# Optimization experiments

Hardware: AMD Instinct MI355X
Metric: run time of the kernel (lower is better)

Reference implementation:

```python
import jax, jax.numpy as jnp
import numpy as np

FIELD = 7  # field_size


def _conv1x1(x, w):
    # x: [b,c,h,w], w: [c_out,c_in] (1x1 conv, no bias)
    return jnp.einsum('bchw,oc->bohw', x, w)


def _patches(x, f):
    # torch unfold with 'same' padding: output [b, c*f*f, h, w], channel-major
    # (feature index = c*f*f + kh*f + kw), matching KAIR extract_image_patches
    # layout for odd f / stride 1 (symmetric pad (f-1)//2).
    return jax.lax.conv_general_dilated_patches(
        x, filter_shape=(f, f), window_strides=(1, 1), padding='SAME',
        dimension_numbers=('NCHW', 'OIHW', 'NCHW'))


def setup_inputs() -> dict:
    key = jax.random.key(0)
    k0, k1, k2, k3, k4 = jax.random.split(key, 5)
    c, ci = 256, 128
    b, h, w = 4, 64, 64
    s = 1.0 / np.sqrt(c)
    si = 1.0 / np.sqrt(ci)
    return {
        'x': jax.random.normal(k0, (b, c, h, w), dtype=jnp.float32),
        'w_phi': jax.random.normal(k1, (ci, c), dtype=jnp.float32) * s,
        'w_theta': jax.random.normal(k2, (ci, c), dtype=jnp.float32) * s,
        'w_g': jax.random.normal(k3, (ci, c), dtype=jnp.float32) * s,
        'w_mask': jax.random.normal(k4, (c, ci), dtype=jnp.float32) * si,
    }


def reference(x, w_phi, w_theta, w_g, w_mask):
    b, c, h, w = x.shape
    ci = w_phi.shape[0]
    f = FIELD
    kk = f * f

    x_phi = _conv1x1(x, w_phi)      # [b,ci,h,w]
    x_g = _conv1x1(x, w_g)          # [b,ci,h,w]
    x_theta = _conv1x1(x, w_theta)  # [b,ci,h,w]

    # theta: unsqueeze(-2) then permute(0,2,4,3,1) -> [b,h,w,1,ci]
    q = jnp.transpose(x_theta, (0, 2, 3, 1))[:, :, :, None, :]

    # phi patches: [b, ci*kk, h, w] reshaped (row-major, faithful to torch
    # reshape of the unfold output) to [b,h,w,ci,kk]
    p_phi = _patches(x_phi, f).reshape(b, h, w, ci, kk)
    scores = jnp.matmul(q, p_phi)                 # [b,h,w,1,kk]
    attn = jax.nn.softmax(scores, axis=1)         # softmax over dim=1 (h), faithful

    p_g = _patches(x_g, f).reshape(b, h, w, kk, ci)
    out = jnp.matmul(attn, p_g)                   # [b,h,w,1,ci]

    # permute(0,4,3,1,2).view(b,ci,h,w)
    y = jnp.transpose(out, (0, 4, 3, 1, 2)).reshape(b, ci, h, w)
    mask = _conv1x1(y, w_mask)                    # [b,c,h,w]
    return mask + x
```

## Files before the change

kernel.cpp:

```cpp
#include <hip/hip_runtime.h>


#define PLANE    5040
#define A_BATCH  645120

typedef __attribute__((ext_vector_type(8))) short short8;
typedef __attribute__((ext_vector_type(4))) float floatx4;

__device__ __forceinline__ float bf2f(unsigned short u) {
    union { unsigned int i; float f; } v; v.i = ((unsigned int)u) << 16; return v.f;
}
__device__ __forceinline__ unsigned short f2bf(float f) {
    union { float f; unsigned int i; } v; v.f = f;
    unsigned int r = v.i + 0x7FFFu + ((v.i >> 16) & 1u);
    return (unsigned short)(r >> 16);
}

__global__ __launch_bounds__(256) void prep_kernel(
    const float* __restrict__ x,
    const float* __restrict__ w_phi,
    const float* __restrict__ w_theta,
    const float* __restrict__ w_g,
    const float* __restrict__ w_mask,
    unsigned short* __restrict__ xp_hi,
    unsigned short* __restrict__ xp_lo,
    unsigned short* __restrict__ w3p_hi,
    unsigned short* __restrict__ w3p_lo,
    unsigned short* __restrict__ wmp_hi,
    unsigned short* __restrict__ wmp_lo,
    uint4* __restrict__ zero_region)
{
    const int tid = threadIdx.x;
    const int bx = blockIdx.x;

    if (bx < 1024) {
        const int b  = bx >> 8;
        const int kt = (bx >> 6) & 3;
        const int pt = bx & 63;
        __shared__ float tile[64][65];
        #pragma unroll
        for (int i = 0; i < 16; ++i) {
            int lin = tid + i * 256;
            int kk = lin >> 6, pp = lin & 63;
            tile[kk][pp] = x[(b * 256 + kt * 64 + kk) * 4096 + pt * 64 + pp];
        }
        __syncthreads();
        #pragma unroll
        for (int i = 0; i < 16; ++i) {
            int lin = tid + i * 256;
            int frag = lin >> 9;
            int idx  = lin & 511;
            int kbL  = frag >> 2;
            int ptL  = frag & 3;
            int j    = idx & 7;
            int n    = (idx >> 3) & 15;
            int quad = idx >> 7;
            float f = tile[kbL * 32 + quad * 8 + j][ptL * 16 + n];
            unsigned short h = f2bf(f);
            int addr = ((b * 8 + kt * 2 + kbL) * 256 + pt * 4 + ptL) * 512 + idx;
            xp_hi[addr] = h;
            xp_lo[addr] = f2bf(f - bf2f(h));
        }
    } else {
        const int wid = (bx - 1024) * 256 + tid;
        for (int e = wid; e < 98304; e += 32768) {
            int frag = e >> 9;
            int idx  = e & 511;
            int nt16 = frag >> 3, kb = frag & 7;
            int j = idx & 7, m = (idx >> 3) & 15, quad = idx >> 7;
            int n = nt16 * 16 + m;
            int k = kb * 32 + quad * 8 + j;
            float v = (n < 128) ? w_phi[n * 256 + k]
                    : (n < 256) ? w_theta[(n - 128) * 256 + k]
                                : w_g[(n - 256) * 256 + k];
            unsigned short h = f2bf(v);
            w3p_hi[e] = h;
            w3p_lo[e] = f2bf(v - bf2f(h));
        }
        {
            int e = wid;
            int frag = e >> 9;
            int idx  = e & 511;
            int ot16 = frag >> 2, kb = frag & 3;
            int j = idx & 7, m = (idx >> 3) & 15, quad = idx >> 7;
            float v = w_mask[(ot16 * 16 + m) * 128 + kb * 32 + quad * 8 + j];
            unsigned short h = f2bf(v);
            wmp_hi[e] = h;
            wmp_lo[e] = f2bf(v - bf2f(h));
        }
        const uint4 z = make_uint4(0u, 0u, 0u, 0u);
        for (int i = wid; i < 645120; i += 32768) zero_region[i] = z;
    }
}

__global__ __launch_bounds__(256) void conv3_mfma_kernel(
    const unsigned short* __restrict__ xp_hi,
    const unsigned short* __restrict__ xp_lo,
    const unsigned short* __restrict__ w3p_hi,
    const unsigned short* __restrict__ w3p_lo,
    unsigned short* __restrict__ A_phi,
    unsigned short* __restrict__ theta_bf,
    unsigned short* __restrict__ A_g)
{
    const int tid = threadIdx.x;
    const int w   = tid >> 6;
    const int ln  = tid & 63;
    const int lm  = ln & 15;
    const int quad = ln >> 4;
    const int bx = blockIdx.x;
    const int nt = blockIdx.y;
    const int b  = blockIdx.z;
    const int nt16a = nt * 8 + w;
    const int nt16b = nt * 8 + 4 + w;
    const int lnofs = ln * 8;

    floatx4 accA[4] = {{0.f,0.f,0.f,0.f},{0.f,0.f,0.f,0.f},
                       {0.f,0.f,0.f,0.f},{0.f,0.f,0.f,0.f}};
    floatx4 accB[4] = {{0.f,0.f,0.f,0.f},{0.f,0.f,0.f,0.f},
                       {0.f,0.f,0.f,0.f},{0.f,0.f,0.f,0.f}};

    #pragma unroll
    for (int kb = 0; kb < 8; ++kb) {
        const int aoffA = (nt16a * 8 + kb) * 512 + lnofs;
        const int aoffB = (nt16b * 8 + kb) * 512 + lnofs;
        const int boff  = ((b * 8 + kb) * 256 + bx * 4) * 512 + lnofs;
        short8 ahA = *reinterpret_cast<const short8*>(w3p_hi + aoffA);
        short8 alA = *reinterpret_cast<const short8*>(w3p_lo + aoffA);
        short8 ahB = *reinterpret_cast<const short8*>(w3p_hi + aoffB);
        short8 alB = *reinterpret_cast<const short8*>(w3p_lo + aoffB);
        short8 bh[4], bl[4];
        #pragma unroll
        for (int ct = 0; ct < 4; ++ct) {
            bh[ct] = *reinterpret_cast<const short8*>(xp_hi + boff + ct * 512);
            bl[ct] = *reinterpret_cast<const short8*>(xp_lo + boff + ct * 512);
        }
        #pragma unroll
        for (int ct = 0; ct < 4; ++ct) {
            accA[ct] = __builtin_amdgcn_mfma_f32_16x16x32_bf16(ahA, bh[ct], accA[ct], 0, 0, 0);
            accA[ct] = __builtin_amdgcn_mfma_f32_16x16x32_bf16(ahA, bl[ct], accA[ct], 0, 0, 0);
            accA[ct] = __builtin_amdgcn_mfma_f32_16x16x32_bf16(alA, bh[ct], accA[ct], 0, 0, 0);
            accB[ct] = __builtin_amdgcn_mfma_f32_16x16x32_bf16(ahB, bh[ct], accB[ct], 0, 0, 0);
            accB[ct] = __builtin_amdgcn_mfma_f32_16x16x32_bf16(ahB, bl[ct], accB[ct], 0, 0, 0);
            accB[ct] = __builtin_amdgcn_mfma_f32_16x16x32_bf16(alB, bh[ct], accB[ct], 0, 0, 0);
        }
    }

    const int py = bx;
    if (nt == 1) {
        #pragma unroll
        for (int ct = 0; ct < 4; ++ct) {
            const int p = bx * 64 + ct * 16 + lm;
            #pragma unroll
            for (int reg = 0; reg < 4; ++reg) {
                const int r = w * 16 + quad * 4 + reg;
                theta_bf[(b * 4096 + p) * 128 + r]      = f2bf(accA[ct][reg]);
                theta_bf[(b * 4096 + p) * 128 + r + 64] = f2bf(accB[ct][reg]);
            }
        }
    } else {
        unsigned short* __restrict__ A = (nt == 0) ? A_phi : A_g;
        #pragma unroll
        for (int ct = 0; ct < 4; ++ct) {
            const int pxx = ct * 16 + lm;
            #pragma unroll
            for (int reg = 0; reg < 4; ++reg) {
                const int r = w * 16 + quad * 4 + reg;
                A[b * A_BATCH + r * PLANE + (py + 3) * 72 + pxx + 4] =
                    f2bf(accA[ct][reg]);
                A[b * A_BATCH + (r + 64) * PLANE + (py + 3) * 72 + pxx + 4] =
                    f2bf(accB[ct][reg]);
            }
        }
    }
}

__global__ __launch_bounds__(256) void scores_kernel(
    const unsigned short* __restrict__ Apad,
    const unsigned short* __restrict__ theta_bf,
    float* __restrict__ scores)
{
    const int w  = threadIdx.x >> 6;
    const int ln = threadIdx.x & 63;
    const int s  = blockIdx.x * 4 + w;
    const int b  = blockIdx.y;

    __shared__ float th[4][128];
    {
        const unsigned short* tb = theta_bf + (b * 4096 + s) * 128;
        th[w][ln]      = bf2f(tb[ln]);
        th[w][ln + 64] = bf2f(tb[ln + 64]);
    }
    __syncthreads();

    const unsigned short* __restrict__ Ab = Apad + b * A_BATCH;

    const int base  = s * 6272;
    const int ch_lo = base >> 12;
    const unsigned B1 = (unsigned)(ch_lo + 1) << 12;
    const unsigned B2 = (unsigned)(ch_lo + 2) << 12;
    const int d1 = (int)B1 - base;
    const int d2 = d1 + 4096;

    int A1 = d1 / 49;
    int A2 = (d1 + 48) / 49;
    int C1 = d2 / 49;        if (C1 > 128) C1 = 128;
    int C2 = (d2 + 48) / 49; if (C2 > 128) C2 = 128;

    unsigned OFFv[3];
    #pragma unroll
    for (int i = 0; i < 3; ++i) {
        int ch = ch_lo + i;
        int c0 = ch / 49; if (c0 > 127) c0 = 127;
        int rr = ch - c0 * 49;
        int kh = rr / 7;
        int kw = rr - kh * 7;
        OFFv[i] = (unsigned)(c0 * PLANE + kh * 72 + kw + 1);
    }

    unsigned F = (unsigned)(base + ln);
    float acc = 0.f;

    {
        const unsigned OFF_ = OFFv[0];
        #pragma unroll 4
        for (int cc = 0; cc < A1; ++cc) {
            unsigned p = F & 4095u;
            unsigned a = OFF_ + p + ((p >> 6) << 3);
            acc = fmaf(th[w][cc], bf2f(Ab[a]), acc);
            F += 49u;
        }
    }
    for (int cc = A1; cc < A2; ++cc) {
        unsigned OFF_ = (F >= B1) ? OFFv[1] : OFFv[0];
        unsigned p = F & 4095u;
        unsigned a = OFF_ + p + ((p >> 6) << 3);
        acc = fmaf(th[w][cc], bf2f(Ab[a]), acc);
        F += 49u;
    }
    {
        const unsigned OFF_ = OFFv[1];
        #pragma unroll 4
        for (int cc = A2; cc < C1; ++cc) {
            unsigned p = F & 4095u;
            unsigned a = OFF_ + p + ((p >> 6) << 3);
            acc = fmaf(th[w][cc], bf2f(Ab[a]), acc);
            F += 49u;
        }
    }
    for (int cc = C1; cc < C2; ++cc) {
        unsigned OFF_ = (F >= B2) ? OFFv[2] : OFFv[1];
        unsigned p = F & 4095u;
        unsigned a = OFF_ + p + ((p >> 6) << 3);
        acc = fmaf(th[w][cc], bf2f(Ab[a]), acc);
        F += 49u;
    }
    {
        const unsigned OFF_ = OFFv[2];
        #pragma unroll 4
        for (int cc = C2; cc < 128; ++cc) {
            unsigned p = F & 4095u;
            unsigned a = OFF_ + p + ((p >> 6) << 3);
            acc = fmaf(th[w][cc], bf2f(Ab[a]), acc);
            F += 49u;
        }
    }

    if (ln < 49) scores[(b * 4096 + s) * 64 + ln] = acc;
}

__global__ __launch_bounds__(256) void softmax_stats_kernel(
    const float* __restrict__ scores,
    float* __restrict__ m_arr,
    float* __restrict__ inv_arr)
{
    const int b = blockIdx.x >> 6;
    const int j = blockIdx.x & 63;
    const int tid = threadIdx.x;
    const int wv = tid >> 6;
    const int ln = tid & 63;

    __shared__ float tile[64][52];

    #pragma unroll
    for (int it = 0; it < 16; ++it) {
        int i = it * 4 + wv;
        if (ln < 49) tile[i][ln] = scores[(b * 4096 + i * 64 + j) * 64 + ln];
    }
    __syncthreads();

    if (tid < 49) {
        float m = -3.4e38f;
        #pragma unroll 8
        for (int i = 0; i < 64; ++i) m = fmaxf(m, tile[i][tid]);
        float sum = 0.f;
        #pragma unroll 8
        for (int i = 0; i < 64; ++i) sum += __expf(tile[i][tid] - m);
        m_arr[(b * 64 + j) * 49 + tid]   = m;
        inv_arr[(b * 64 + j) * 49 + tid] = 1.f / sum;
    }
}

__global__ __launch_bounds__(256) void aggregate_kernel(
    const float* __restrict__ scores,
    const float* __restrict__ m_arr,
    const float* __restrict__ inv_arr,
    const unsigned short* __restrict__ Apad,
    unsigned short* __restrict__ y_p)
{
    const int pix = threadIdx.x >> 7;
    const int cc  = threadIdx.x & 127;
    const int s   = blockIdx.x * 2 + pix;
    const int b   = blockIdx.y;

    __shared__ float at[2][52];
    if (cc < 49) {
        const int j = s & 63;
        float sc = scores[(b * 4096 + s) * 64 + cc];
        float m  = m_arr[(b * 64 + j) * 49 + cc];
        float iv = inv_arr[(b * 64 + j) * 49 + cc];
        at[pix][cc] = __expf(sc - m) * iv;
    }
    __syncthreads();

    const unsigned short* __restrict__ Ab = Apad + b * A_BATCH;

    const int base  = s * 6272;
    const int ch_lo = base >> 12;
    const unsigned B1 = (unsigned)(ch_lo + 1) << 12;
    const unsigned B2 = (unsigned)(ch_lo + 2) << 12;
    const int d1 = (int)B1 - base;
    const int d2 = d1 + 4096;

    int A1 = d1 >> 7;
    int A2 = (d1 + 127) >> 7;
    int C1 = d2 >> 7;          if (C1 > 49) C1 = 49;
    int C2 = (d2 + 127) >> 7;  if (C2 > 49) C2 = 49;
    if (A1 > 49) A1 = 49;
    if (A2 > 49) A2 = 49;

    unsigned OFFv[3];
    #pragma unroll
    for (int i = 0; i < 3; ++i) {
        int ch = ch_lo + i;
        int c0 = ch / 49; if (c0 > 127) c0 = 127;
        int rr = ch - c0 * 49;
        int kh = rr / 7;
        int kw = rr - kh * 7;
        OFFv[i] = (unsigned)(c0 * PLANE + kh * 72 + kw + 1);
    }

    unsigned F = (unsigned)(base + cc);
    float acc = 0.f;

    {
        const unsigned OFF_ = OFFv[0];
        #pragma unroll 4
        for (int t = 0; t < A1; ++t) {
            unsigned p = F & 4095u;
            unsigned a = OFF_ + p + ((p >> 6) << 3);
            acc = fmaf(at[pix][t], bf2f(Ab[a]), acc);
            F += 128u;
        }
    }
    for (int t = A1; t < A2; ++t) {
        unsigned OFF_ = (F >= B1) ? OFFv[1] : OFFv[0];
        unsigned p = F & 4095u;
        unsigned a = OFF_ + p + ((p >> 6) << 3);
        acc = fmaf(at[pix][t], bf2f(Ab[a]), acc);
        F += 128u;
    }
    {
        const unsigned OFF_ = OFFv[1];
        #pragma unroll 4
        for (int t = A2; t < C1; ++t) {
            unsigned p = F & 4095u;
            unsigned a = OFF_ + p + ((p >> 6) << 3);
            acc = fmaf(at[pix][t], bf2f(Ab[a]), acc);
            F += 128u;
        }
    }
    for (int t = C1; t < C2; ++t) {
        unsigned OFF_ = (F >= B2) ? OFFv[2] : OFFv[1];
        unsigned p = F & 4095u;
        unsigned a = OFF_ + p + ((p >> 6) << 3);
        acc = fmaf(at[pix][t], bf2f(Ab[a]), acc);
        F += 128u;
    }
    {
        const unsigned OFF_ = OFFv[2];
        for (int t = C2; t < 49; ++t) {
            unsigned p = F & 4095u;
            unsigned a = OFF_ + p + ((p >> 6) << 3);
            acc = fmaf(at[pix][t], bf2f(Ab[a]), acc);
            F += 128u;
        }
    }

    const int kb = cc >> 5, k32 = cc & 31;
    const int quad = k32 >> 3, j = k32 & 7;
    const int pt16 = s >> 4, n = s & 15;
    y_p[((b * 4 + kb) * 256 + pt16) * 512 + (quad * 16 + n) * 8 + j] = f2bf(acc);
}

__global__ __launch_bounds__(256) void maskconv_mfma_kernel(
    const float* __restrict__ x,
    const unsigned short* __restrict__ wmp_hi,
    const unsigned short* __restrict__ wmp_lo,
    const unsigned short* __restrict__ y_p,
    float* __restrict__ out)
{
    const int tid = threadIdx.x;
    const int w   = tid >> 6;
    const int ln  = tid & 63;
    const int lm  = ln & 15;
    const int quad = ln >> 4;
    const int bx = blockIdx.x;
    const int ot = blockIdx.y;
    const int b  = blockIdx.z;
    const int ot16a = ot * 8 + w;
    const int ot16b = ot * 8 + 4 + w;
    const int lnofs = ln * 8;

    floatx4 accA[4] = {{0.f,0.f,0.f,0.f},{0.f,0.f,0.f,0.f},
                       {0.f,0.f,0.f,0.f},{0.f,0.f,0.f,0.f}};
    floatx4 accB[4] = {{0.f,0.f,0.f,0.f},{0.f,0.f,0.f,0.f},
                       {0.f,0.f,0.f,0.f},{0.f,0.f,0.f,0.f}};

    #pragma unroll
    for (int kb = 0; kb < 4; ++kb) {
        const int aoffA = (ot16a * 4 + kb) * 512 + lnofs;
        const int aoffB = (ot16b * 4 + kb) * 512 + lnofs;
        const int boff  = ((b * 4 + kb) * 256 + bx * 4) * 512 + lnofs;
        short8 ahA = *reinterpret_cast<const short8*>(wmp_hi + aoffA);
        short8 alA = *reinterpret_cast<const short8*>(wmp_lo + aoffA);
        short8 ahB = *reinterpret_cast<const short8*>(wmp_hi + aoffB);
        short8 alB = *reinterpret_cast<const short8*>(wmp_lo + aoffB);
        short8 bf[4];
        #pragma unroll
        for (int ct = 0; ct < 4; ++ct)
            bf[ct] = *reinterpret_cast<const short8*>(y_p + boff + ct * 512);
        #pragma unroll
        for (int ct = 0; ct < 4; ++ct) {
            accA[ct] = __builtin_amdgcn_mfma_f32_16x16x32_bf16(ahA, bf[ct], accA[ct], 0, 0, 0);
            accA[ct] = __builtin_amdgcn_mfma_f32_16x16x32_bf16(alA, bf[ct], accA[ct], 0, 0, 0);
            accB[ct] = __builtin_amdgcn_mfma_f32_16x16x32_bf16(ahB, bf[ct], accB[ct], 0, 0, 0);
            accB[ct] = __builtin_amdgcn_mfma_f32_16x16x32_bf16(alB, bf[ct], accB[ct], 0, 0, 0);
        }
    }

    #pragma unroll
    for (int ct = 0; ct < 4; ++ct) {
        const int p = bx * 64 + ct * 16 + lm;
        #pragma unroll
        for (int reg = 0; reg < 4; ++reg) {
            const int oA = ot * 128 + w * 16 + quad * 4 + reg;
            const int ofsA = (b * 256 + oA) * 4096 + p;
            out[ofsA] = accA[ct][reg] + x[ofsA];
            const int ofsB = ofsA + 64 * 4096;
            out[ofsB] = accB[ct][reg] + x[ofsB];
        }
    }
}

extern "C" void kernel_launch(void* const* d_in, const int* in_sizes, int n_in,
                              void* d_out, int out_size, void* d_ws, size_t ws_size,
                              hipStream_t stream) {
    const float* x       = (const float*)d_in[0];
    const float* w_phi   = (const float*)d_in[1];
    const float* w_theta = (const float*)d_in[2];
    const float* w_g     = (const float*)d_in[3];
    const float* w_mask  = (const float*)d_in[4];

    float* out_f = (float*)d_out;

    unsigned short* ws_u  = (unsigned short*)d_ws;
    unsigned short* A_phi = ws_u;
    unsigned short* A_g   = ws_u + 2580480;
    unsigned short* y_p   = ws_u + 5160960;
    unsigned short* th_u  = ws_u + 7258112;
    float*          sc_f  = (float*)(ws_u + 9355264);
    unsigned short* xph   = ws_u + 11452416;
    unsigned short* xpl   = ws_u + 15646720;
    unsigned short* w3ph  = ws_u + 19841024;
    unsigned short* w3pl  = ws_u + 19939328;
    unsigned short* wmph  = ws_u + 20037632;
    unsigned short* wmpl  = ws_u + 20070400;
    float*          m_f   = (float*)(ws_u + 20103168);
    float*          inv_f = (float*)(ws_u + 20128256);

    hipLaunchKernelGGL(prep_kernel, dim3(1152), dim3(256), 0, stream,
                       x, w_phi, w_theta, w_g, w_mask,
                       xph, xpl, w3ph, w3pl, wmph, wmpl, (uint4*)A_phi);
    hipLaunchKernelGGL(conv3_mfma_kernel, dim3(64, 3, 4), dim3(256), 0, stream,
                       xph, xpl, w3ph, w3pl, A_phi, th_u, A_g);
    hipLaunchKernelGGL(scores_kernel, dim3(1024, 4), dim3(256), 0, stream,
                       A_phi, th_u, sc_f);
    hipLaunchKernelGGL(softmax_stats_kernel, dim3(256), dim3(256), 0, stream,
                       sc_f, m_f, inv_f);
    hipLaunchKernelGGL(aggregate_kernel, dim3(2048, 4), dim3(256), 0, stream,
                       sc_f, m_f, inv_f, A_g, y_p);
    hipLaunchKernelGGL(maskconv_mfma_kernel, dim3(64, 2, 4), dim3(256), 0, stream,
                       x, wmph, wmpl, y_p, out_f);
}
```

Measured before the change: 177.6 us.

## Compute all three projections per block to reuse loaded input tiles

The three-projection 1x1 conv kernel now has each block compute phi, theta and g together for 32 pixels, instead of one projection for 64 pixels. Each loaded x tile (hi/lo bf16 split) is reused across all three weight sets, so activation reads drop to a third. The grid changes from 64x3x4 to 128x4 blocks. The cost is more weight loads per block and more accumulator registers (12 floatx4 instead of 8).

```diff
diff --git a/kernel.cpp b/kernel.cpp
--- a/kernel.cpp
+++ b/kernel.cpp
@@ -108,68 +108,73 @@
     const int lm  = ln & 15;
     const int quad = ln >> 4;
     const int bx = blockIdx.x;
-    const int nt = blockIdx.y;
-    const int b  = blockIdx.z;
-    const int nt16a = nt * 8 + w;
-    const int nt16b = nt * 8 + 4 + w;
+    const int b  = blockIdx.y;
     const int lnofs = ln * 8;
 
-    floatx4 accA[4] = {{0.f,0.f,0.f,0.f},{0.f,0.f,0.f,0.f},
-                       {0.f,0.f,0.f,0.f},{0.f,0.f,0.f,0.f}};
-    floatx4 accB[4] = {{0.f,0.f,0.f,0.f},{0.f,0.f,0.f,0.f},
-                       {0.f,0.f,0.f,0.f},{0.f,0.f,0.f,0.f}};
+    floatx4 acc[3][2][2];
+    #pragma unroll
+    for (int nt = 0; nt < 3; ++nt)
+        #pragma unroll
+        for (int tl = 0; tl < 2; ++tl)
+            #pragma unroll
+            for (int ct = 0; ct < 2; ++ct)
+                acc[nt][tl][ct] = (floatx4){0.f, 0.f, 0.f, 0.f};
 
     #pragma unroll
     for (int kb = 0; kb < 8; ++kb) {
-        const int aoffA = (nt16a * 8 + kb) * 512 + lnofs;
-        const int aoffB = (nt16b * 8 + kb) * 512 + lnofs;
-        const int boff  = ((b * 8 + kb) * 256 + bx * 4) * 512 + lnofs;
-        short8 ahA = *reinterpret_cast<const short8*>(w3p_hi + aoffA);
-        short8 alA = *reinterpret_cast<const short8*>(w3p_lo + aoffA);
-        short8 ahB = *reinterpret_cast<const short8*>(w3p_hi + aoffB);
-        short8 alB = *reinterpret_cast<const short8*>(w3p_lo + aoffB);
-        short8 bh[4], bl[4];
-        #pragma unroll
-        for (int ct = 0; ct < 4; ++ct) {
+        const int boff = ((b * 8 + kb) * 256 + bx * 2) * 512 + lnofs;
+        short8 bh[2], bl[2];
+        #pragma unroll
+        for (int ct = 0; ct < 2; ++ct) {
             bh[ct] = *reinterpret_cast<const short8*>(xp_hi + boff + ct * 512);
             bl[ct] = *reinterpret_cast<const short8*>(xp_lo + boff + ct * 512);
         }
         #pragma unroll
-        for (int ct = 0; ct < 4; ++ct) {
-            accA[ct] = __builtin_amdgcn_mfma_f32_16x16x32_bf16(ahA, bh[ct], accA[ct], 0, 0, 0);
-            accA[ct] = __builtin_amdgcn_mfma_f32_16x16x32_bf16(ahA, bl[ct], accA[ct], 0, 0, 0);
-            accA[ct] = __builtin_amdgcn_mfma_f32_16x16x32_bf16(alA, bh[ct], accA[ct], 0, 0, 0);
-            accB[ct] = __builtin_amdgcn_mfma_f32_16x16x32_bf16(ahB, bh[ct], accB[ct], 0, 0, 0);
-            accB[ct] = __builtin_amdgcn_mfma_f32_16x16x32_bf16(ahB, bl[ct], accB[ct], 0, 0, 0);
-            accB[ct] = __builtin_amdgcn_mfma_f32_16x16x32_bf16(alB, bh[ct], accB[ct], 0, 0, 0);
-        }
-    }
-
-    const int py = bx;
-    if (nt == 1) {
-        #pragma unroll
-        for (int ct = 0; ct < 4; ++ct) {
-            const int p = bx * 64 + ct * 16 + lm;
+        for (int nt = 0; nt < 3; ++nt) {
+            const int nt16a = nt * 8 + w;
+            const int nt16b = nt * 8 + 4 + w;
+            const int aoffA = (nt16a * 8 + kb) * 512 + lnofs;
+            const int aoffB = (nt16b * 8 + kb) * 512 + lnofs;
+            short8 ahA = *reinterpret_cast<const short8*>(w3p_hi + aoffA);
+            short8 alA = *reinterpret_cast<const short8*>(w3p_lo + aoffA);
+            short8 ahB = *reinterpret_cast<const short8*>(w3p_hi + aoffB);
+            short8 alB = *reinterpret_cast<const short8*>(w3p_lo + aoffB);
             #pragma unroll
-            for (int reg = 0; reg < 4; ++reg) {
-                const int r = w * 16 + quad * 4 + reg;
-                theta_bf[(b * 4096 + p) * 128 + r]      = f2bf(accA[ct][reg]);
-                theta_bf[(b * 4096 + p) * 128 + r + 64] = f2bf(accB[ct][reg]);
+            for (int ct = 0; ct < 2; ++ct) {
+                acc[nt][0][ct] = __builtin_amdgcn_mfma_f32_16x16x32_bf16(ahA, bh[ct], acc[nt][0][ct], 0, 0, 0);
+                acc[nt][0][ct] = __builtin_amdgcn_mfma_f32_16x16x32_bf16(ahA, bl[ct], acc[nt][0][ct], 0, 0, 0);
+                acc[nt][0][ct] = __builtin_amdgcn_mfma_f32_16x16x32_bf16(alA, bh[ct], acc[nt][0][ct], 0, 0, 0);
+                acc[nt][1][ct] = __builtin_amdgcn_mfma_f32_16x16x32_bf16(ahB, bh[ct], acc[nt][1][ct], 0, 0, 0);
+                acc[nt][1][ct] = __builtin_amdgcn_mfma_f32_16x16x32_bf16(ahB, bl[ct], acc[nt][1][ct], 0, 0, 0);
+                acc[nt][1][ct] = __builtin_amdgcn_mfma_f32_16x16x32_bf16(alB, bh[ct], acc[nt][1][ct], 0, 0, 0);
             }
         }
-    } else {
-        unsigned short* __restrict__ A = (nt == 0) ? A_phi : A_g;
-        #pragma unroll
-        for (int ct = 0; ct < 4; ++ct) {
-            const int pxx = ct * 16 + lm;
-            #pragma unroll
-            for (int reg = 0; reg < 4; ++reg) {
-                const int r = w * 16 + quad * 4 + reg;
-                A[b * A_BATCH + r * PLANE + (py + 3) * 72 + pxx + 4] =
-                    f2bf(accA[ct][reg]);
-                A[b * A_BATCH + (r + 64) * PLANE + (py + 3) * 72 + pxx + 4] =
-                    f2bf(accB[ct][reg]);
-            }
+    }
+
+    const int py   = bx >> 1;
+    const int px32 = (bx & 1) * 32;
+
+    #pragma unroll
+    for (int ct = 0; ct < 2; ++ct) {
+        const int p = bx * 32 + ct * 16 + lm;
+        #pragma unroll
+        for (int reg = 0; reg < 4; ++reg) {
+            const int r = w * 16 + quad * 4 + reg;
+            theta_bf[(b * 4096 + p) * 128 + r]      = f2bf(acc[1][0][ct][reg]);
+            theta_bf[(b * 4096 + p) * 128 + r + 64] = f2bf(acc[1][1][ct][reg]);
+        }
+    }
+    #pragma unroll
+    for (int ct = 0; ct < 2; ++ct) {
+        const int pxx = px32 + ct * 16 + lm;
+        const int pbase = (py + 3) * 72 + pxx + 4;
+        #pragma unroll
+        for (int reg = 0; reg < 4; ++reg) {
+            const int r = w * 16 + quad * 4 + reg;
+            A_phi[b * A_BATCH + r * PLANE + pbase]        = f2bf(acc[0][0][ct][reg]);
+            A_phi[b * A_BATCH + (r + 64) * PLANE + pbase] = f2bf(acc[0][1][ct][reg]);
+            A_g[b * A_BATCH + r * PLANE + pbase]          = f2bf(acc[2][0][ct][reg]);
+            A_g[b * A_BATCH + (r + 64) * PLANE + pbase]   = f2bf(acc[2][1][ct][reg]);
         }
     }
 }
@@ -491,7 +496,7 @@
     hipLaunchKernelGGL(prep_kernel, dim3(1152), dim3(256), 0, stream,
                        x, w_phi, w_theta, w_g, w_mask,
                        xph, xpl, w3ph, w3pl, wmph, wmpl, (uint4*)A_phi);
-    hipLaunchKernelGGL(conv3_mfma_kernel, dim3(64, 3, 4), dim3(256), 0, stream,
+    hipLaunchKernelGGL(conv3_mfma_kernel, dim3(128, 4), dim3(256), 0, stream,
                        xph, xpl, w3ph, w3pl, A_phi, th_u, A_g);
     hipLaunchKernelGGL(scores_kernel, dim3(1024, 4), dim3(256), 0, stream,
                        A_phi, th_u, sc_f);
```

After: 183.0 us. 1.03x slower.

## Fuse attention aggregation and mask 1x1 conv into one kernel via LDS

Applied to the files above, without the earlier changes.

Merges the aggregate kernel and the mask-conv MFMA kernel into a single kernel. Each 512-thread block aggregates 32 pixels into an LDS tile in MFMA operand layout, then runs the full 256-output-channel mask conv on those pixels. This removes one launch and the global write and read of the y_p intermediate. The cost is fewer blocks (512 instead of 8192 and 512), more serial aggregation work per block, and the mask weights being reloaded by every block.

```diff
diff --git a/kernel.cpp b/kernel.cpp
--- a/kernel.cpp
+++ b/kernel.cpp
@@ -300,147 +300,155 @@
     }
 }
 
-__global__ __launch_bounds__(256) void aggregate_kernel(
+__global__ __launch_bounds__(512) void agg_mask_kernel(
     const float* __restrict__ scores,
     const float* __restrict__ m_arr,
     const float* __restrict__ inv_arr,
     const unsigned short* __restrict__ Apad,
-    unsigned short* __restrict__ y_p)
-{
-    const int pix = threadIdx.x >> 7;
-    const int cc  = threadIdx.x & 127;
-    const int s   = blockIdx.x * 2 + pix;
-    const int b   = blockIdx.y;
-
-    __shared__ float at[2][52];
-    if (cc < 49) {
-        const int j = s & 63;
-        float sc = scores[(b * 4096 + s) * 64 + cc];
-        float m  = m_arr[(b * 64 + j) * 49 + cc];
-        float iv = inv_arr[(b * 64 + j) * 49 + cc];
-        at[pix][cc] = __expf(sc - m) * iv;
-    }
-    __syncthreads();
-
-    const unsigned short* __restrict__ Ab = Apad + b * A_BATCH;
-
-    const int base  = s * 6272;
-    const int ch_lo = base >> 12;
-    const unsigned B1 = (unsigned)(ch_lo + 1) << 12;
-    const unsigned B2 = (unsigned)(ch_lo + 2) << 12;
-    const int d1 = (int)B1 - base;
-    const int d2 = d1 + 4096;
-
-    int A1 = d1 >> 7;
-    int A2 = (d1 + 127) >> 7;
-    int C1 = d2 >> 7;          if (C1 > 49) C1 = 49;
-    int C2 = (d2 + 127) >> 7;  if (C2 > 49) C2 = 49;
-    if (A1 > 49) A1 = 49;
-    if (A2 > 49) A2 = 49;
-
-    unsigned OFFv[3];
-    #pragma unroll
-    for (int i = 0; i < 3; ++i) {
-        int ch = ch_lo + i;
-        int c0 = ch / 49; if (c0 > 127) c0 = 127;
-        int rr = ch - c0 * 49;
-        int kh = rr / 7;
-        int kw = rr - kh * 7;
-        OFFv[i] = (unsigned)(c0 * PLANE + kh * 72 + kw + 1);
-    }
-
-    unsigned F = (unsigned)(base + cc);
-    float acc = 0.f;
-
-    {
-        const unsigned OFF_ = OFFv[0];
-        #pragma unroll 4
-        for (int t = 0; t < A1; ++t) {
-            unsigned p = F & 4095u;
-            unsigned a = OFF_ + p + ((p >> 6) << 3);
-            acc = fmaf(at[pix][t], bf2f(Ab[a]), acc);
-            F += 128u;
-        }
-    }
-    for (int t = A1; t < A2; ++t) {
-        unsigned OFF_ = (F >= B1) ? OFFv[1] : OFFv[0];
-        unsigned p = F & 4095u;
-        unsigned a = OFF_ + p + ((p >> 6) << 3);
-        acc = fmaf(at[pix][t], bf2f(Ab[a]), acc);
-        F += 128u;
-    }
-    {
-        const unsigned OFF_ = OFFv[1];
-        #pragma unroll 4
-        for (int t = A2; t < C1; ++t) {
-            unsigned p = F & 4095u;
-            unsigned a = OFF_ + p + ((p >> 6) << 3);
-            acc = fmaf(at[pix][t], bf2f(Ab[a]), acc);
-            F += 128u;
-        }
-    }
-    for (int t = C1; t < C2; ++t) {
-        unsigned OFF_ = (F >= B2) ? OFFv[2] : OFFv[1];
-        unsigned p = F & 4095u;
-        unsigned a = OFF_ + p + ((p >> 6) << 3);
-        acc = fmaf(at[pix][t], bf2f(Ab[a]), acc);
-        F += 128u;
-    }
-    {
-        const unsigned OFF_ = OFFv[2];
-        for (int t = C2; t < 49; ++t) {
-            unsigned p = F & 4095u;
-            unsigned a = OFF_ + p + ((p >> 6) << 3);
-            acc = fmaf(at[pix][t], bf2f(Ab[a]), acc);
-            F += 128u;
-        }
-    }
-
-    const int kb = cc >> 5, k32 = cc & 31;
-    const int quad = k32 >> 3, j = k32 & 7;
-    const int pt16 = s >> 4, n = s & 15;
-    y_p[((b * 4 + kb) * 256 + pt16) * 512 + (quad * 16 + n) * 8 + j] = f2bf(acc);
-}
-
-__global__ __launch_bounds__(256) void maskconv_mfma_kernel(
-    const float* __restrict__ x,
     const unsigned short* __restrict__ wmp_hi,
     const unsigned short* __restrict__ wmp_lo,
-    const unsigned short* __restrict__ y_p,
+    const float* __restrict__ x,
     float* __restrict__ out)
 {
     const int tid = threadIdx.x;
-    const int w   = tid >> 6;
-    const int ln  = tid & 63;
-    const int lm  = ln & 15;
+    const int blk = blockIdx.x;
+    const int b   = blockIdx.y;
+    const int P0  = blk * 32;
+
+    __shared__ float at_l[32][52];
+    __shared__ unsigned short y_lds[8 * 512];
+
+    const int j0 = P0 & 63;
+    #pragma unroll
+    for (int it = 0; it < 4; ++it) {
+        int idx = tid + it * 512;
+        int lp = idx >> 6;
+        int t  = idx & 63;
+        if (t < 49) {
+            const int s = P0 + lp;
+            const int j = j0 + lp;
+            float sc = scores[(b * 4096 + s) * 64 + t];
+            float m  = m_arr[(b * 64 + j) * 49 + t];
+            float iv = inv_arr[(b * 64 + j) * 49 + t];
+            at_l[lp][t] = __expf(sc - m) * iv;
+        }
+    }
+    __syncthreads();
+
+    const unsigned short* __restrict__ Ab = Apad + b * A_BATCH;
+    const int pq = tid >> 7;
+    const int cc = tid & 127;
+
+    #pragma unroll
+    for (int rep = 0; rep < 8; ++rep) {
+        const int lp = rep * 4 + pq;
+        const int s  = P0 + lp;
+
+        const int base  = s * 6272;
+        const int ch_lo = base >> 12;
+        const unsigned B1 = (unsigned)(ch_lo + 1) << 12;
+        const unsigned B2 = (unsigned)(ch_lo + 2) << 12;
+        const int d1 = (int)B1 - base;
+        const int d2 = d1 + 4096;
+
+        int A1 = d1 >> 7;
+        int A2 = (d1 + 127) >> 7;
+        int C1 = d2 >> 7;          if (C1 > 49) C1 = 49;
+        int C2 = (d2 + 127) >> 7;  if (C2 > 49) C2 = 49;
+        if (A1 > 49) A1 = 49;
+        if (A2 > 49) A2 = 49;
+
+        unsigned OFFv[3];
+        #pragma unroll
+        for (int i = 0; i < 3; ++i) {
+            int ch = ch_lo + i;
+            int c0 = ch / 49; if (c0 > 127) c0 = 127;
+            int rr = ch - c0 * 49;
+            int kh = rr / 7;
+            int kw = rr - kh * 7;
+            OFFv[i] = (unsigned)(c0 * PLANE + kh * 72 + kw + 1);
+        }
+
+        unsigned F = (unsigned)(base + cc);
+        float acc = 0.f;
+
+        {
+            const unsigned OFF_ = OFFv[0];
+            #pragma unroll 4
+            for (int t = 0; t < A1; ++t) {
+                unsigned p = F & 4095u;
+                unsigned a = OFF_ + p + ((p >> 6) << 3);
+                acc = fmaf(at_l[lp][t], bf2f(Ab[a]), acc);
+                F += 128u;
+            }
+        }
+        for (int t = A1; t < A2; ++t) {
+            unsigned OFF_ = (F >= B1) ? OFFv[1] : OFFv[0];
+            unsigned p = F & 4095u;
+            unsigned a = OFF_ + p + ((p >> 6) << 3);
+            acc = fmaf(at_l[lp][t], bf2f(Ab[a]), acc);
+            F += 128u;
+        }
+        {
+            const unsigned OFF_ = OFFv[1];
+            #pragma unroll 4
+            for (int t = A2; t < C1; ++t) {
+                unsigned p = F & 4095u;
+                unsigned a = OFF_ + p + ((p >> 6) << 3);
+                acc = fmaf(at_l[lp][t], bf2f(Ab[a]), acc);
+                F += 128u;
+            }
+        }
+        for (int t = C1; t < C2; ++t) {
+            unsigned OFF_ = (F >= B2) ? OFFv[2] : OFFv[1];
+            unsigned p = F & 4095u;
+            unsigned a = OFF_ + p + ((p >> 6) << 3);
+            acc = fmaf(at_l[lp][t], bf2f(Ab[a]), acc);
+            F += 128u;
+        }
+        {
+            const unsigned OFF_ = OFFv[2];
+            for (int t = C2; t < 49; ++t) {
+                unsigned p = F & 4095u;
+                unsigned a = OFF_ + p + ((p >> 6) << 3);
+                acc = fmaf(at_l[lp][t], bf2f(Ab[a]), acc);
+                F += 128u;
+            }
+        }
+
+        const int kb = cc >> 5, k32 = cc & 31;
+        const int quad = k32 >> 3, jx = k32 & 7;
+        const int ct = lp >> 4, n = lp & 15;
+        y_lds[(kb * 2 + ct) * 512 + (quad * 16 + n) * 8 + jx] = f2bf(acc);
+    }
+    __syncthreads();
+
+    const int w    = tid >> 6;
+    const int ln   = tid & 63;
+    const int lm   = ln & 15;
     const int quad = ln >> 4;
-    const int bx = blockIdx.x;
-    const int ot = blockIdx.y;
-    const int b  = blockIdx.z;
-    const int ot16a = ot * 8 + w;
-    const int ot16b = ot * 8 + 4 + w;
     const int lnofs = ln * 8;
-
-    floatx4 accA[4] = {{0.f,0.f,0.f,0.f},{0.f,0.f,0.f,0.f},
-                       {0.f,0.f,0.f,0.f},{0.f,0.f,0.f,0.f}};
-    floatx4 accB[4] = {{0.f,0.f,0.f,0.f},{0.f,0.f,0.f,0.f},
-                       {0.f,0.f,0.f,0.f},{0.f,0.f,0.f,0.f}};
+    const int ot16a = w;
+    const int ot16b = w + 8;
+
+    floatx4 accA[2] = {{0.f,0.f,0.f,0.f},{0.f,0.f,0.f,0.f}};
+    floatx4 accB[2] = {{0.f,0.f,0.f,0.f},{0.f,0.f,0.f,0.f}};
 
     #pragma unroll
     for (int kb = 0; kb < 4; ++kb) {
         const int aoffA = (ot16a * 4 + kb) * 512 + lnofs;
         const int aoffB = (ot16b * 4 + kb) * 512 + lnofs;
-        const int boff  = ((b * 4 + kb) * 256 + bx * 4) * 512 + lnofs;
         short8 ahA = *reinterpret_cast<const short8*>(wmp_hi + aoffA);
         short8 alA = *reinterpret_cast<const short8*>(wmp_lo + aoffA);
         short8 ahB = *reinterpret_cast<const short8*>(wmp_hi + aoffB);
         short8 alB = *reinterpret_cast<const short8*>(wmp_lo + aoffB);
-        short8 bf[4];
-        #pragma unroll
-        for (int ct = 0; ct < 4; ++ct)
-            bf[ct] = *reinterpret_cast<const short8*>(y_p + boff + ct * 512);
-        #pragma unroll
-        for (int ct = 0; ct < 4; ++ct) {
+        short8 bf[2];
+        #pragma unroll
+        for (int ct = 0; ct < 2; ++ct)
+            bf[ct] = *reinterpret_cast<const short8*>(
+                y_lds + (kb * 2 + ct) * 512 + lnofs);
+        #pragma unroll
+        for (int ct = 0; ct < 2; ++ct) {
             accA[ct] = __builtin_amdgcn_mfma_f32_16x16x32_bf16(ahA, bf[ct], accA[ct], 0, 0, 0);
             accA[ct] = __builtin_amdgcn_mfma_f32_16x16x32_bf16(alA, bf[ct], accA[ct], 0, 0, 0);
             accB[ct] = __builtin_amdgcn_mfma_f32_16x16x32_bf16(ahB, bf[ct], accB[ct], 0, 0, 0);
@@ -449,14 +457,14 @@
     }
 
     #pragma unroll
-    for (int ct = 0; ct < 4; ++ct) {
-        const int p = bx * 64 + ct * 16 + lm;
+    for (int ct = 0; ct < 2; ++ct) {
+        const int p = P0 + ct * 16 + lm;
         #pragma unroll
         for (int reg = 0; reg < 4; ++reg) {
-            const int oA = ot * 128 + w * 16 + quad * 4 + reg;
+            const int oA = w * 16 + quad * 4 + reg;
             const int ofsA = (b * 256 + oA) * 4096 + p;
             out[ofsA] = accA[ct][reg] + x[ofsA];
-            const int ofsB = ofsA + 64 * 4096;
+            const int ofsB = ofsA + 128 * 4096;
             out[ofsB] = accB[ct][reg] + x[ofsB];
         }
     }
@@ -476,7 +484,6 @@
     unsigned short* ws_u  = (unsigned short*)d_ws;
     unsigned short* A_phi = ws_u;
     unsigned short* A_g   = ws_u + 2580480;
-    unsigned short* y_p   = ws_u + 5160960;
     unsigned short* th_u  = ws_u + 7258112;
     float*          sc_f  = (float*)(ws_u + 9355264);
     unsigned short* xph   = ws_u + 11452416;
@@ -497,8 +504,6 @@
                        A_phi, th_u, sc_f);
     hipLaunchKernelGGL(softmax_stats_kernel, dim3(256), dim3(256), 0, stream,
                        sc_f, m_f, inv_f);
-    hipLaunchKernelGGL(aggregate_kernel, dim3(2048, 4), dim3(256), 0, stream,
-                       sc_f, m_f, inv_f, A_g, y_p);
-    hipLaunchKernelGGL(maskconv_mfma_kernel, dim3(64, 2, 4), dim3(256), 0, stream,
-                       x, wmph, wmpl, y_p, out_f);
-}
+    hipLaunchKernelGGL(agg_mask_kernel, dim3(128, 4), dim3(512), 0, stream,
+                       sc_f, m_f, inv_f, A_g, wmph, wmpl, x, out_f);
+}
```

After: 174.3 us. About the same (-1.9%).
